# Kernel tuning notes

Hardware: AMD Instinct MI355X
Metric: run time of the kernel (lower is better)

Reference implementation:

```python
import jax, jax.numpy as jnp
import numpy as np
import math

D = 1024          # d_model = dk = dv
B = 2             # batch
T = 2048          # seq_len
F = 2 * D         # RFF feature dim
RFF_SCALE = math.sqrt(2.0 / D)
EPS = 1e-6


def setup_inputs() -> dict:
    key = jax.random.key(0)
    ks = jax.random.split(key, 6)
    s = 1.0 / math.sqrt(D)
    return {
        "x": jax.random.normal(ks[0], (B, T, D), dtype=jnp.float32),
        "Wq": jax.random.normal(ks[1], (D, D), dtype=jnp.float32) * s,
        "Wk": jax.random.normal(ks[2], (D, D), dtype=jnp.float32) * s,
        "Wv": jax.random.normal(ks[3], (D, D), dtype=jnp.float32) * s,
        "Wo": jax.random.normal(ks[4], (D, D), dtype=jnp.float32) * s,
        "omega": jax.random.normal(ks[5], (D, D), dtype=jnp.float32) * 0.5,
    }


def _rff(x, omega):
    # phi(x) = sqrt(2/m) * [cos(x @ omega), sin(x @ omega)]
    proj = x @ omega                       # (B, T, D)
    return RFF_SCALE * jnp.concatenate([jnp.cos(proj), jnp.sin(proj)], axis=-1)


def _linear_attention(Q_phi, K_phi, V):
    # Causal linear-attention recurrence over time via lax.scan.
    # S_t = S_{t-1} + phi(K_t)^T V_t ; Z_t = Z_{t-1} + phi(K_t)
    # gamma_t = (phi(Q_t) S_t) / (phi(Q_t) Z_t + eps)
    b, t, f = Q_phi.shape
    dv = V.shape[-1]
    S0 = jnp.zeros((b, f, dv), Q_phi.dtype)
    Z0 = jnp.zeros((b, f), Q_phi.dtype)

    def step(carry, inp):
        S, Z = carry
        kp, v, qp = inp                        # (B,F), (B,Dv), (B,F)
        S = S + kp[:, :, None] * v[:, None, :]  # outer-product memory update
        Z = Z + kp
        num = jnp.einsum('bf,bfd->bd', qp, S)
        den = jnp.einsum('bf,bf->b', qp, Z)
        gamma = num / (den[:, None] + EPS)
        return (S, Z), gamma

    # time-major inputs for scan
    xs = (jnp.swapaxes(K_phi, 0, 1), jnp.swapaxes(V, 0, 1), jnp.swapaxes(Q_phi, 0, 1))
    _, ys = jax.lax.scan(step, (S0, Z0), xs)   # ys: (T, B, Dv)
    return jnp.swapaxes(ys, 0, 1)              # (B, T, Dv)


def reference(x, Wq, Wk, Wv, Wo, omega):
    Q = x @ Wq
    K = x @ Wk
    V = x @ Wv
    Q_phi = _rff(Q, omega)
    K_phi = _rff(K, omega)
    y = _linear_attention(Q_phi, K_phi, V)
    return y @ Wo
```

## Files before the change

### kernel.cpp

```cpp
#include <hip/hip_runtime.h>

#define D_ 1024
#define B_ 2
#define T_ 2048
#define F_ 2048
#define CHUNK 512
#define NCHUNK 4
#define EPS_ 1e-6f
#define RSCALE 0.044194173824159216f

template<int EPI>
__global__ __launch_bounds__(256)
void sgemm128(const float* __restrict__ A, const float* __restrict__ B,
              float* __restrict__ C, int M, int N, int K, int ldc) {
    __shared__ float As[16][132];
    __shared__ float Bs[16][132];
    const int tid = threadIdx.x;
    const int bm = blockIdx.x * 128;
    const int bn = blockIdx.y * 128;
    const int tx = tid & 15, ty = tid >> 4;
    float acc[2][2][4][4] = {};
    const float* Ab = A + (size_t)bm * K;
    const float* Bb = B + bn;

    for (int k0 = 0; k0 < K; k0 += 16) {
#pragma unroll
        for (int l = 0; l < 2; ++l) {
            int idx = tid + l * 256;
            int r  = idx >> 2;
            int c4 = (idx & 3) << 2;
            float4 a = *(const float4*)(Ab + (size_t)r * K + k0 + c4);
            As[c4 + 0][r] = a.x; As[c4 + 1][r] = a.y;
            As[c4 + 2][r] = a.z; As[c4 + 3][r] = a.w;
            int rb = idx >> 5;
            int cb = (idx & 31) << 2;
            *(float4*)(&Bs[rb][cb]) = *(const float4*)(Bb + (size_t)(k0 + rb) * N + cb);
        }
        __syncthreads();
#pragma unroll
        for (int k = 0; k < 16; ++k) {
            float4 a0 = *(float4*)(&As[k][ty * 4]);
            float4 a1 = *(float4*)(&As[k][64 + ty * 4]);
            float4 b0 = *(float4*)(&Bs[k][tx * 4]);
            float4 b1 = *(float4*)(&Bs[k][64 + tx * 4]);
            float av[2][4] = {{a0.x, a0.y, a0.z, a0.w}, {a1.x, a1.y, a1.z, a1.w}};
            float bv[2][4] = {{b0.x, b0.y, b0.z, b0.w}, {b1.x, b1.y, b1.z, b1.w}};
#pragma unroll
            for (int ri = 0; ri < 2; ++ri)
#pragma unroll
                for (int i = 0; i < 4; ++i)
#pragma unroll
                    for (int ci = 0; ci < 2; ++ci)
#pragma unroll
                        for (int j = 0; j < 4; ++j)
                            acc[ri][ci][i][j] = fmaf(av[ri][i], bv[ci][j], acc[ri][ci][i][j]);
        }
        __syncthreads();
    }

#pragma unroll
    for (int ri = 0; ri < 2; ++ri)
#pragma unroll
        for (int i = 0; i < 4; ++i) {
            int R = bm + ri * 64 + ty * 4 + i;
#pragma unroll
            for (int ci = 0; ci < 2; ++ci) {
                int col = bn + ci * 64 + tx * 4;
                if (EPI == 0) {
                    float4 v = make_float4(acc[ri][ci][i][0], acc[ri][ci][i][1],
                                           acc[ri][ci][i][2], acc[ri][ci][i][3]);
                    *(float4*)(&C[(size_t)R * ldc + col]) = v;
                } else {
                    float cs[4], sn[4];
#pragma unroll
                    for (int j = 0; j < 4; ++j)
                        __sincosf(acc[ri][ci][i][j], &sn[j], &cs[j]);
                    float4 cv = make_float4(RSCALE * cs[0], RSCALE * cs[1],
                                            RSCALE * cs[2], RSCALE * cs[3]);
                    float4 sv = make_float4(RSCALE * sn[0], RSCALE * sn[1],
                                            RSCALE * sn[2], RSCALE * sn[3]);
                    *(float4*)(&C[(size_t)R * ldc + col])      = cv;
                    *(float4*)(&C[(size_t)R * ldc + col + D_]) = sv;
                }
            }
        }
}

__global__ __launch_bounds__(256)
void pall_kernel(const float* __restrict__ Qp, const float* __restrict__ Kp,
                 float* __restrict__ P) {
    const int tt = blockIdx.x >> 4, ts = blockIdx.x & 15;
    const int c = blockIdx.y, b = blockIdx.z;
    const int t0 = tt * 32, s0 = ts * 32;
    float* Pc = P + (((size_t)b * NCHUNK + c) * CHUNK) * CHUNK;
    const int tid = threadIdx.x;
    if (tt < ts) {
        int r = tid >> 3, c4 = (tid & 7) << 2;
        *(float4*)(&Pc[(size_t)(t0 + r) * CHUNK + s0 + c4]) = make_float4(0, 0, 0, 0);
        return;
    }
    __shared__ float Qs[32][36];
    __shared__ float Ks[32][36];
    const int tx = tid & 15, ty = tid >> 4;
    float acc[2][2] = {};
    const float* Qb = Qp + ((size_t)b * T_ + c * CHUNK + t0) * F_;
    const float* Kb = Kp + ((size_t)b * T_ + c * CHUNK + s0) * F_;
    for (int f0 = 0; f0 < F_; f0 += 32) {
        int r = tid >> 3, c4 = (tid & 7) << 2;
        *(float4*)(&Qs[r][c4]) = *(const float4*)(Qb + (size_t)r * F_ + f0 + c4);
        *(float4*)(&Ks[r][c4]) = *(const float4*)(Kb + (size_t)r * F_ + f0 + c4);
        __syncthreads();
#pragma unroll
        for (int k = 0; k < 32; ++k) {
            float q0 = Qs[ty * 2][k],     q1 = Qs[ty * 2 + 1][k];
            float k0v = Ks[tx * 2][k],    k1v = Ks[tx * 2 + 1][k];
            acc[0][0] = fmaf(q0, k0v, acc[0][0]);
            acc[0][1] = fmaf(q0, k1v, acc[0][1]);
            acc[1][0] = fmaf(q1, k0v, acc[1][0]);
            acc[1][1] = fmaf(q1, k1v, acc[1][1]);
        }
        __syncthreads();
    }
#pragma unroll
    for (int i = 0; i < 2; ++i)
#pragma unroll
        for (int j = 0; j < 2; ++j) {
            int t = t0 + ty * 2 + i, s = s0 + tx * 2 + j;
            Pc[(size_t)t * CHUNK + s] = (s <= t) ? acc[i][j] : 0.0f;
        }
}

__global__ __launch_bounds__(256)
void csum_kernel(const float* __restrict__ Kp, float* __restrict__ Zpre) {
    const int f = blockIdx.x * 256 + threadIdx.x;
    const int c = blockIdx.y, b = blockIdx.z;
    const float* base = Kp + ((size_t)b * T_ + c * CHUNK) * F_ + f;
    float acc = 0.f;
    for (int s = 0; s < CHUNK; ++s) acc += base[(size_t)s * F_];
    Zpre[((size_t)b * NCHUNK + c) * F_ + f] = acc;
}

__global__ __launch_bounds__(256)
void zprefix_kernel(float* __restrict__ Zpre) {
    const int f = blockIdx.x * 256 + threadIdx.x;
    const int b = blockIdx.y;
    float run = 0.f;
    for (int c = 0; c < NCHUNK; ++c) {
        size_t idx = ((size_t)b * NCHUNK + c) * F_ + f;
        float v = Zpre[idx];
        Zpre[idx] = run;
        run += v;
    }
}

__global__ __launch_bounds__(256)
void den_kernel(const float* __restrict__ Qp, const float* __restrict__ Zpre,
                const float* __restrict__ P, float* __restrict__ den) {
    const int b = blockIdx.y;
    const int w = threadIdx.x >> 6, lane = threadIdx.x & 63;
    const int t = blockIdx.x * 4 + w;
    const int c = t / CHUNK, tin = t % CHUNK;
    const float* q = Qp + ((size_t)b * T_ + t) * F_;
    const float* z = Zpre + ((size_t)b * NCHUNK + c) * F_;
    float acc = 0.f;
    for (int f = lane; f < F_; f += 64) acc = fmaf(q[f], z[f], acc);
    const float* prow = P + (((size_t)b * NCHUNK + c) * CHUNK + tin) * CHUNK;
    for (int s = lane; s < CHUNK; s += 64) acc += prow[s];
#pragma unroll
    for (int off = 32; off; off >>= 1) acc += __shfl_down(acc, off);
    if (lane == 0) den[(size_t)b * T_ + t] = acc;
}

__global__ __launch_bounds__(256)
void intra_kernel(const float* __restrict__ P, const float* __restrict__ V,
                  float* __restrict__ G) {
    const int rt = blockIdx.x >> 4, ct = blockIdx.x & 15;
    const int c = blockIdx.y, b = blockIdx.z;
    const float* Pa = P + (((size_t)b * NCHUNK + c) * CHUNK + rt * 64) * CHUNK;
    const float* Vb = V + ((size_t)b * T_ + c * CHUNK) * D_ + ct * 64;
    float* Gb = G + ((size_t)b * T_ + c * CHUNK + rt * 64) * D_ + ct * 64;
    __shared__ float As[16][68];
    __shared__ float Bs[16][68];
    const int tid = threadIdx.x, tx = tid & 15, ty = tid >> 4;
    float acc[4][4] = {};
    for (int k0 = 0; k0 < CHUNK; k0 += 16) {
        int r = tid >> 2, c4 = (tid & 3) << 2;
        float4 a = *(const float4*)(Pa + (size_t)r * CHUNK + k0 + c4);
        As[c4 + 0][r] = a.x; As[c4 + 1][r] = a.y;
        As[c4 + 2][r] = a.z; As[c4 + 3][r] = a.w;
        int rb = tid >> 4, cb = (tid & 15) << 2;
        *(float4*)(&Bs[rb][cb]) = *(const float4*)(Vb + (size_t)(k0 + rb) * D_ + cb);
        __syncthreads();
#pragma unroll
        for (int k = 0; k < 16; ++k) {
            float4 av = *(float4*)(&As[k][ty * 4]);
            float4 bv = *(float4*)(&Bs[k][tx * 4]);
            float aa[4] = {av.x, av.y, av.z, av.w};
            float bb[4] = {bv.x, bv.y, bv.z, bv.w};
#pragma unroll
            for (int i = 0; i < 4; ++i)
#pragma unroll
                for (int j = 0; j < 4; ++j)
                    acc[i][j] = fmaf(aa[i], bb[j], acc[i][j]);
        }
        __syncthreads();
    }
#pragma unroll
    for (int i = 0; i < 4; ++i)
        *(float4*)(&Gb[(size_t)(ty * 4 + i) * D_ + tx * 4]) =
            make_float4(acc[i][0], acc[i][1], acc[i][2], acc[i][3]);
}

__global__ __launch_bounds__(256)
void gamma_kernel(const float* __restrict__ Qp, const float* __restrict__ S,
                  const float* __restrict__ den, float* __restrict__ G, int c) {
    const int rt = blockIdx.x >> 4, ct = blockIdx.x & 15;
    const int b = blockIdx.y;
    const int row0 = c * CHUNK + rt * 32;
    const float* Qb = Qp + ((size_t)b * T_ + row0) * F_;
    const float* Sb = S + (size_t)b * F_ * D_ + ct * 64;
    float* Gb = G + ((size_t)b * T_ + row0) * D_ + ct * 64;
    const float* db = den + (size_t)b * T_ + row0;
    __shared__ float As[32][36];
    __shared__ float Bs[32][68];
    const int tid = threadIdx.x, tx = tid & 15, ty = tid >> 4;
    float acc[2][4] = {};
    for (int k0 = 0; k0 < F_; k0 += 32) {
        int r = tid >> 3, c4 = (tid & 7) << 2;
        float4 a = *(const float4*)(Qb + (size_t)r * F_ + k0 + c4);
        As[c4 + 0][r] = a.x; As[c4 + 1][r] = a.y;
        As[c4 + 2][r] = a.z; As[c4 + 3][r] = a.w;
#pragma unroll
        for (int l = 0; l < 2; ++l) {
            int idx = tid + l * 256;
            int rb = idx >> 4, cb = (idx & 15) << 2;
            *(float4*)(&Bs[rb][cb]) = *(const float4*)(Sb + (size_t)(k0 + rb) * D_ + cb);
        }
        __syncthreads();
#pragma unroll
        for (int k = 0; k < 32; ++k) {
            float a0 = As[k][ty * 2], a1 = As[k][ty * 2 + 1];
            float4 bv = *(float4*)(&Bs[k][tx * 4]);
            acc[0][0] = fmaf(a0, bv.x, acc[0][0]);
            acc[0][1] = fmaf(a0, bv.y, acc[0][1]);
            acc[0][2] = fmaf(a0, bv.z, acc[0][2]);
            acc[0][3] = fmaf(a0, bv.w, acc[0][3]);
            acc[1][0] = fmaf(a1, bv.x, acc[1][0]);
            acc[1][1] = fmaf(a1, bv.y, acc[1][1]);
            acc[1][2] = fmaf(a1, bv.z, acc[1][2]);
            acc[1][3] = fmaf(a1, bv.w, acc[1][3]);
        }
        __syncthreads();
    }
#pragma unroll
    for (int i = 0; i < 2; ++i) {
        int r = ty * 2 + i;
        float dd = db[r] + EPS_;
        float4 g = *(float4*)(&Gb[(size_t)r * D_ + tx * 4]);
        g.x = (acc[i][0] + g.x) / dd;
        g.y = (acc[i][1] + g.y) / dd;
        g.z = (acc[i][2] + g.z) / dd;
        g.w = (acc[i][3] + g.w) / dd;
        *(float4*)(&Gb[(size_t)r * D_ + tx * 4]) = g;
    }
}

__global__ __launch_bounds__(256)
void supd_kernel(const float* __restrict__ Kp, const float* __restrict__ V,
                 float* __restrict__ S, int c) {
    const int ft = blockIdx.x >> 4, dt = blockIdx.x & 15;
    const int b = blockIdx.y;
    const float* Kb = Kp + ((size_t)b * T_ + c * CHUNK) * F_ + ft * 64;
    const float* Vb = V + ((size_t)b * T_ + c * CHUNK) * D_ + dt * 64;
    float* Sb = S + (size_t)b * F_ * D_ + (size_t)ft * 64 * D_ + dt * 64;
    __shared__ float Ks[16][68];
    __shared__ float Vs[16][68];
    const int tid = threadIdx.x, tx = tid & 15, ty = tid >> 4;
    float acc[4][4] = {};
    for (int k0 = 0; k0 < CHUNK; k0 += 16) {
        int rb = tid >> 4, cb = (tid & 15) << 2;
        *(float4*)(&Ks[rb][cb]) = *(const float4*)(Kb + (size_t)(k0 + rb) * F_ + cb);
        *(float4*)(&Vs[rb][cb]) = *(const float4*)(Vb + (size_t)(k0 + rb) * D_ + cb);
        __syncthreads();
#pragma unroll
        for (int k = 0; k < 16; ++k) {
            float4 av = *(float4*)(&Ks[k][ty * 4]);
            float4 bv = *(float4*)(&Vs[k][tx * 4]);
            float aa[4] = {av.x, av.y, av.z, av.w};
            float bb[4] = {bv.x, bv.y, bv.z, bv.w};
#pragma unroll
            for (int i = 0; i < 4; ++i)
#pragma unroll
                for (int j = 0; j < 4; ++j)
                    acc[i][j] = fmaf(aa[i], bb[j], acc[i][j]);
        }
        __syncthreads();
    }
#pragma unroll
    for (int i = 0; i < 4; ++i) {
        float4* p = (float4*)(&Sb[(size_t)(ty * 4 + i) * D_ + tx * 4]);
        float4 s = *p;
        s.x += acc[i][0]; s.y += acc[i][1]; s.z += acc[i][2]; s.w += acc[i][3];
        *p = s;
    }
}

extern "C" void kernel_launch(void* const* d_in, const int* in_sizes, int n_in,
                              void* d_out, int out_size, void* d_ws, size_t ws_size,
                              hipStream_t stream) {
    const float* x     = (const float*)d_in[0];
    const float* Wq    = (const float*)d_in[1];
    const float* Wk    = (const float*)d_in[2];
    const float* Wv    = (const float*)d_in[3];
    const float* Wo    = (const float*)d_in[4];
    const float* omega = (const float*)d_in[5];
    float* out = (float*)d_out;
    float* ws = (float*)d_ws;

    float* Wqo   = ws;
    float* Wko   = Wqo + 1048576;
    float* V     = Wko + 1048576;
    float* Qphi  = V + 4194304;
    float* Kphi  = Qphi + 8388608;
    float* gamma = Kphi + 8388608;
    float* S     = gamma + 4194304;
    float* P     = S + 4194304;
    float* den   = P + 2097152;
    float* Zpre  = den + 4096;

    const int M = B_ * T_;

    hipMemsetAsync(S, 0, (size_t)B_ * F_ * D_ * sizeof(float), stream);

    sgemm128<0><<<dim3(8, 8), 256, 0, stream>>>(Wq, omega, Wqo, D_, D_, D_, D_);
    sgemm128<0><<<dim3(8, 8), 256, 0, stream>>>(Wk, omega, Wko, D_, D_, D_, D_);

    sgemm128<0><<<dim3(M / 128, 8), 256, 0, stream>>>(x, Wv, V, M, D_, D_, D_);
    sgemm128<1><<<dim3(M / 128, 8), 256, 0, stream>>>(x, Wqo, Qphi, M, D_, D_, F_);
    sgemm128<1><<<dim3(M / 128, 8), 256, 0, stream>>>(x, Wko, Kphi, M, D_, D_, F_);

    csum_kernel<<<dim3(F_ / 256, NCHUNK, B_), 256, 0, stream>>>(Kphi, Zpre);
    zprefix_kernel<<<dim3(F_ / 256, B_), 256, 0, stream>>>(Zpre);

    pall_kernel<<<dim3(256, NCHUNK, B_), 256, 0, stream>>>(Qphi, Kphi, P);
    den_kernel<<<dim3(T_ / 4, B_), 256, 0, stream>>>(Qphi, Zpre, P, den);
    intra_kernel<<<dim3(128, NCHUNK, B_), 256, 0, stream>>>(P, V, gamma);

    for (int c = 0; c < NCHUNK; ++c) {
        gamma_kernel<<<dim3(256, B_), 256, 0, stream>>>(Qphi, S, den, gamma, c);
        supd_kernel<<<dim3(512, B_), 256, 0, stream>>>(Kphi, V, S, c);
    }

    sgemm128<0><<<dim3(M / 128, 8), 256, 0, stream>>>(gamma, Wo, out, M, D_, D_, D_);
}
```

Baseline: 1.845 ms.

## Replace chunked recurrence with full causal-masked quadratic attention using split-bf16 MFMA

Drops the chunked S-state recurrence (intra, gamma and state-update kernels) and computes attention directly as a causal-masked phi(Q)phi(K)^T matrix multiplied by V. This runs on bf16 MFMA with a hi/lo split (three products) to approximate fp32 accuracy, and the output projection by Wo moves to the same MFMA path. Inputs are converted and transposed into split-bf16 buffers, and the work is processed per batch in a host loop. In exchange it adds conversion and transpose passes, does more FLOPs than the linear form for the full causal matrix, and gives up some precision compared with true fp32.

```diff
diff --git a/kernel.cpp b/kernel.cpp
--- a/kernel.cpp
+++ b/kernel.cpp
@@ -1,4 +1,10 @@
 #include <hip/hip_runtime.h>
+
+typedef unsigned short u16;
+typedef __attribute__((ext_vector_type(8))) short s8v;
+typedef __attribute__((ext_vector_type(4))) float f4v;
+typedef __attribute__((ext_vector_type(4))) unsigned short us4v;
+typedef __attribute__((ext_vector_type(8))) unsigned short us8v;
 
 #define D_ 1024
 #define B_ 2
@@ -8,6 +14,22 @@
 #define NCHUNK 4
 #define EPS_ 1e-6f
 #define RSCALE 0.044194173824159216f
+
+__device__ __forceinline__ u16 bf16h(float a) {
+    unsigned u = __float_as_uint(a);
+    return (u16)((u + 0x7fffu + ((u >> 16) & 1u)) >> 16);
+}
+__device__ __forceinline__ float bf2f(u16 h) {
+    return __uint_as_float(((unsigned)h) << 16);
+}
+__device__ __forceinline__ void bsplit2(float a, u16& h, u16& l) {
+    h = bf16h(a);
+    l = bf16h(a - bf2f(h));
+}
+
+#define GLOAD16(gp, lp) __builtin_amdgcn_global_load_lds( \
+    (const __attribute__((address_space(1))) unsigned int*)(gp), \
+    (__attribute__((address_space(3))) unsigned int*)(lp), 16, 0, 0)
 
 template<int EPI>
 __global__ __launch_bounds__(256)
@@ -171,138 +193,148 @@
     if (lane == 0) den[(size_t)b * T_ + t] = acc;
 }
 
-__global__ __launch_bounds__(256)
-void intra_kernel(const float* __restrict__ P, const float* __restrict__ V,
-                  float* __restrict__ G) {
-    const int rt = blockIdx.x >> 4, ct = blockIdx.x & 15;
-    const int c = blockIdx.y, b = blockIdx.z;
-    const float* Pa = P + (((size_t)b * NCHUNK + c) * CHUNK + rt * 64) * CHUNK;
-    const float* Vb = V + ((size_t)b * T_ + c * CHUNK) * D_ + ct * 64;
-    float* Gb = G + ((size_t)b * T_ + c * CHUNK + rt * 64) * D_ + ct * 64;
-    __shared__ float As[16][68];
-    __shared__ float Bs[16][68];
-    const int tid = threadIdx.x, tx = tid & 15, ty = tid >> 4;
-    float acc[4][4] = {};
-    for (int k0 = 0; k0 < CHUNK; k0 += 16) {
-        int r = tid >> 2, c4 = (tid & 3) << 2;
-        float4 a = *(const float4*)(Pa + (size_t)r * CHUNK + k0 + c4);
-        As[c4 + 0][r] = a.x; As[c4 + 1][r] = a.y;
-        As[c4 + 2][r] = a.z; As[c4 + 3][r] = a.w;
-        int rb = tid >> 4, cb = (tid & 15) << 2;
-        *(float4*)(&Bs[rb][cb]) = *(const float4*)(Vb + (size_t)(k0 + rb) * D_ + cb);
-        __syncthreads();
-#pragma unroll
-        for (int k = 0; k < 16; ++k) {
-            float4 av = *(float4*)(&As[k][ty * 4]);
-            float4 bv = *(float4*)(&Bs[k][tx * 4]);
-            float aa[4] = {av.x, av.y, av.z, av.w};
-            float bb[4] = {bv.x, bv.y, bv.z, bv.w};
+template<int EPI>
+__global__ __launch_bounds__(256)
+void mgemm2(const u16* __restrict__ A0, const u16* __restrict__ A1,
+            const u16* __restrict__ B0, const u16* __restrict__ B1,
+            int K, float* __restrict__ Cf, u16* __restrict__ O0,
+            u16* __restrict__ O1, const float* __restrict__ dptr, int ldo) {
+    __shared__ u16 lds[4 * 4096];
+    const int tid = threadIdx.x;
+    const int bm = blockIdx.x * 128, bn = blockIdx.y * 128;
+
+    if (EPI == 3 && bm + 128 <= bn) {
+        us8v zz = {0, 0, 0, 0, 0, 0, 0, 0};
+#pragma unroll
+        for (int i = 0; i < 8; ++i) {
+            int j = i * 256 + tid;
+            int r = j >> 4, c8 = (j & 15) * 8;
+            size_t o = (size_t)(bm + r) * ldo + bn + c8;
+            *(us8v*)&O0[o] = zz;
+            *(us8v*)&O1[o] = zz;
+        }
+        return;
+    }
+
+    const int kend = (EPI == 5) ? (bm + 128 < K ? bm + 128 : K) : K;
+
+    const int wv = tid >> 6, lane = tid & 63;
+    const int wr = (wv >> 1) * 64, wc = (wv & 1) * 64;
+    const int lr = lane & 15, kb = lane >> 4;
+
+    f4v acc[4][4] = {};
+
+    const int sr0 = tid >> 2, sc0 = (tid & 3) * 8;
+    const int sl0 = tid * 8, sl1 = (tid + 256) * 8;
+
+    for (int k0 = 0; k0 < kend; k0 += 32) {
+        size_t ga0 = (size_t)(bm + sr0) * K + k0 + sc0;
+        size_t ga1 = ga0 + (size_t)64 * K;
+        size_t gb0 = (size_t)(bn + sr0) * K + k0 + sc0;
+        size_t gb1 = gb0 + (size_t)64 * K;
+        GLOAD16(A0 + ga0, lds + 0 * 4096 + sl0);
+        GLOAD16(A0 + ga1, lds + 0 * 4096 + sl1);
+        GLOAD16(A1 + ga0, lds + 1 * 4096 + sl0);
+        GLOAD16(A1 + ga1, lds + 1 * 4096 + sl1);
+        GLOAD16(B0 + gb0, lds + 2 * 4096 + sl0);
+        GLOAD16(B0 + gb1, lds + 2 * 4096 + sl1);
+        GLOAD16(B1 + gb0, lds + 3 * 4096 + sl0);
+        GLOAD16(B1 + gb1, lds + 3 * 4096 + sl1);
+        __syncthreads();
+
+        constexpr int TA[3] = {0, 0, 1};
+        constexpr int TB[3] = {0, 1, 0};
+#pragma unroll
+        for (int t = 0; t < 3; ++t) {
+            const u16* la = lds + TA[t] * 4096;
+            const u16* lb = lds + (2 + TB[t]) * 4096;
+            s8v af[4], bfr[4];
+#pragma unroll
+            for (int i = 0; i < 4; ++i) {
+                af[i]  = *(const s8v*)&la[(wr + i * 16 + lr) * 32 + kb * 8];
+                bfr[i] = *(const s8v*)&lb[(wc + i * 16 + lr) * 32 + kb * 8];
+            }
 #pragma unroll
             for (int i = 0; i < 4; ++i)
 #pragma unroll
                 for (int j = 0; j < 4; ++j)
-                    acc[i][j] = fmaf(aa[i], bb[j], acc[i][j]);
-        }
-        __syncthreads();
-    }
-#pragma unroll
-    for (int i = 0; i < 4; ++i)
-        *(float4*)(&Gb[(size_t)(ty * 4 + i) * D_ + tx * 4]) =
-            make_float4(acc[i][0], acc[i][1], acc[i][2], acc[i][3]);
-}
-
-__global__ __launch_bounds__(256)
-void gamma_kernel(const float* __restrict__ Qp, const float* __restrict__ S,
-                  const float* __restrict__ den, float* __restrict__ G, int c) {
-    const int rt = blockIdx.x >> 4, ct = blockIdx.x & 15;
-    const int b = blockIdx.y;
-    const int row0 = c * CHUNK + rt * 32;
-    const float* Qb = Qp + ((size_t)b * T_ + row0) * F_;
-    const float* Sb = S + (size_t)b * F_ * D_ + ct * 64;
-    float* Gb = G + ((size_t)b * T_ + row0) * D_ + ct * 64;
-    const float* db = den + (size_t)b * T_ + row0;
-    __shared__ float As[32][36];
-    __shared__ float Bs[32][68];
-    const int tid = threadIdx.x, tx = tid & 15, ty = tid >> 4;
-    float acc[2][4] = {};
-    for (int k0 = 0; k0 < F_; k0 += 32) {
-        int r = tid >> 3, c4 = (tid & 7) << 2;
-        float4 a = *(const float4*)(Qb + (size_t)r * F_ + k0 + c4);
-        As[c4 + 0][r] = a.x; As[c4 + 1][r] = a.y;
-        As[c4 + 2][r] = a.z; As[c4 + 3][r] = a.w;
-#pragma unroll
-        for (int l = 0; l < 2; ++l) {
-            int idx = tid + l * 256;
-            int rb = idx >> 4, cb = (idx & 15) << 2;
-            *(float4*)(&Bs[rb][cb]) = *(const float4*)(Sb + (size_t)(k0 + rb) * D_ + cb);
-        }
-        __syncthreads();
-#pragma unroll
-        for (int k = 0; k < 32; ++k) {
-            float a0 = As[k][ty * 2], a1 = As[k][ty * 2 + 1];
-            float4 bv = *(float4*)(&Bs[k][tx * 4]);
-            acc[0][0] = fmaf(a0, bv.x, acc[0][0]);
-            acc[0][1] = fmaf(a0, bv.y, acc[0][1]);
-            acc[0][2] = fmaf(a0, bv.z, acc[0][2]);
-            acc[0][3] = fmaf(a0, bv.w, acc[0][3]);
-            acc[1][0] = fmaf(a1, bv.x, acc[1][0]);
-            acc[1][1] = fmaf(a1, bv.y, acc[1][1]);
-            acc[1][2] = fmaf(a1, bv.z, acc[1][2]);
-            acc[1][3] = fmaf(a1, bv.w, acc[1][3]);
-        }
-        __syncthreads();
-    }
-#pragma unroll
-    for (int i = 0; i < 2; ++i) {
-        int r = ty * 2 + i;
-        float dd = db[r] + EPS_;
-        float4 g = *(float4*)(&Gb[(size_t)r * D_ + tx * 4]);
-        g.x = (acc[i][0] + g.x) / dd;
-        g.y = (acc[i][1] + g.y) / dd;
-        g.z = (acc[i][2] + g.z) / dd;
-        g.w = (acc[i][3] + g.w) / dd;
-        *(float4*)(&Gb[(size_t)r * D_ + tx * 4]) = g;
-    }
-}
-
-__global__ __launch_bounds__(256)
-void supd_kernel(const float* __restrict__ Kp, const float* __restrict__ V,
-                 float* __restrict__ S, int c) {
-    const int ft = blockIdx.x >> 4, dt = blockIdx.x & 15;
-    const int b = blockIdx.y;
-    const float* Kb = Kp + ((size_t)b * T_ + c * CHUNK) * F_ + ft * 64;
-    const float* Vb = V + ((size_t)b * T_ + c * CHUNK) * D_ + dt * 64;
-    float* Sb = S + (size_t)b * F_ * D_ + (size_t)ft * 64 * D_ + dt * 64;
-    __shared__ float Ks[16][68];
-    __shared__ float Vs[16][68];
-    const int tid = threadIdx.x, tx = tid & 15, ty = tid >> 4;
-    float acc[4][4] = {};
-    for (int k0 = 0; k0 < CHUNK; k0 += 16) {
-        int rb = tid >> 4, cb = (tid & 15) << 2;
-        *(float4*)(&Ks[rb][cb]) = *(const float4*)(Kb + (size_t)(k0 + rb) * F_ + cb);
-        *(float4*)(&Vs[rb][cb]) = *(const float4*)(Vb + (size_t)(k0 + rb) * D_ + cb);
-        __syncthreads();
-#pragma unroll
-        for (int k = 0; k < 16; ++k) {
-            float4 av = *(float4*)(&Ks[k][ty * 4]);
-            float4 bv = *(float4*)(&Vs[k][tx * 4]);
-            float aa[4] = {av.x, av.y, av.z, av.w};
-            float bb[4] = {bv.x, bv.y, bv.z, bv.w};
-#pragma unroll
-            for (int i = 0; i < 4; ++i)
-#pragma unroll
-                for (int j = 0; j < 4; ++j)
-                    acc[i][j] = fmaf(aa[i], bb[j], acc[i][j]);
-        }
-        __syncthreads();
-    }
+                    acc[i][j] = __builtin_amdgcn_mfma_f32_16x16x32_bf16(
+                        af[i], bfr[j], acc[i][j], 0, 0, 0);
+        }
+        __syncthreads();
+    }
+
+    const int rbase = bm + wr + kb * 4;
+    const int cbase = bn + wc + lr;
 #pragma unroll
     for (int i = 0; i < 4; ++i) {
-        float4* p = (float4*)(&Sb[(size_t)(ty * 4 + i) * D_ + tx * 4]);
-        float4 s = *p;
-        s.x += acc[i][0]; s.y += acc[i][1]; s.z += acc[i][2]; s.w += acc[i][3];
-        *p = s;
-    }
+        const int R0 = rbase + i * 16;
+#pragma unroll
+        for (int j = 0; j < 4; ++j) {
+            const int Cc = cbase + j * 16;
+            f4v v = acc[i][j];
+            if (EPI == 0) {
+#pragma unroll
+                for (int q = 0; q < 4; ++q)
+                    Cf[(size_t)(R0 + q) * ldo + Cc] = v[q];
+            } else if (EPI == 3) {
+#pragma unroll
+                for (int q = 0; q < 4; ++q) {
+                    int t = R0 + q;
+                    float val = (Cc <= t) ? v[q] : 0.0f;
+                    u16 h, l; bsplit2(val, h, l);
+                    size_t o = (size_t)t * ldo + Cc;
+                    O0[o] = h; O1[o] = l;
+                }
+            } else if (EPI == 5) {
+#pragma unroll
+                for (int q = 0; q < 4; ++q) {
+                    float g = v[q] / (dptr[R0 + q] + EPS_);
+                    u16 h, l; bsplit2(g, h, l);
+                    size_t o = (size_t)(R0 + q) * ldo + Cc;
+                    O0[o] = h; O1[o] = l;
+                }
+            }
+        }
+    }
+}
+
+__global__ __launch_bounds__(256)
+void convk2(const float* __restrict__ in, u16* __restrict__ o0,
+            u16* __restrict__ o1, int n4) {
+    int i = blockIdx.x * 256 + threadIdx.x;
+    if (i >= n4) return;
+    float4 v = ((const float4*)in)[i];
+    us4v p0, p1;
+    float vv[4] = {v.x, v.y, v.z, v.w};
+#pragma unroll
+    for (int q = 0; q < 4; ++q) {
+        u16 h, l; bsplit2(vv[q], h, l);
+        p0[q] = h; p1[q] = l;
+    }
+    ((us4v*)o0)[i] = p0;
+    ((us4v*)o1)[i] = p1;
+}
+
+__global__ __launch_bounds__(256)
+void tpc(const float* __restrict__ in, u16* __restrict__ oh,
+         u16* __restrict__ ol, int inW, int outW) {
+    __shared__ float t[32][33];
+    const int r = threadIdx.x >> 3, c4 = (threadIdx.x & 7) << 2;
+    const int row0 = blockIdx.y * 32, col0 = blockIdx.x * 32;
+    float4 v = *(const float4*)&in[(size_t)(row0 + r) * inW + col0 + c4];
+    t[r][c4 + 0] = v.x; t[r][c4 + 1] = v.y;
+    t[r][c4 + 2] = v.z; t[r][c4 + 3] = v.w;
+    __syncthreads();
+    us4v h4, l4;
+#pragma unroll
+    for (int i = 0; i < 4; ++i) {
+        u16 h, l; bsplit2(t[c4 + i][r], h, l);
+        h4[i] = h; l4[i] = l;
+    }
+    size_t o = (size_t)(col0 + r) * outW + row0 + c4;
+    *(us4v*)&oh[o] = h4;
+    *(us4v*)&ol[o] = l4;
 }
 
 extern "C" void kernel_launch(void* const* d_in, const int* in_sizes, int n_in,
@@ -315,41 +347,53 @@
     const float* Wo    = (const float*)d_in[4];
     const float* omega = (const float*)d_in[5];
     float* out = (float*)d_out;
-    float* ws = (float*)d_ws;
-
-    float* Wqo   = ws;
-    float* Wko   = Wqo + 1048576;
-    float* V     = Wko + 1048576;
-    float* Qphi  = V + 4194304;
-    float* Kphi  = Qphi + 8388608;
-    float* gamma = Kphi + 8388608;
-    float* S     = gamma + 4194304;
-    float* P     = S + 4194304;
-    float* den   = P + 2097152;
-    float* Zpre  = den + 4096;
-
-    const int M = B_ * T_;
-
-    hipMemsetAsync(S, 0, (size_t)B_ * F_ * D_ * sizeof(float), stream);
+
+    char* WS = (char*)d_ws;
+    float* Wqo = (float*)(WS + 0);
+    float* Wko = (float*)(WS + 4194304);
+    u16*  WoTh = (u16*)(WS + 8388608);
+    u16*  WoTl = (u16*)(WS + 10485760);
+    float* den = (float*)(WS + 12582912);
+    float* Zpre = (float*)(WS + 12599296);
+    float* Qf  = (float*)(WS + 13631488);
+    float* Kf  = (float*)(WS + 30408704);
+    float* Vf  = (float*)(WS + 47185920);
+    float* Pd  = (float*)(WS + 55574528);
+    u16* Qph = (u16*)(WS + 59768832);
+    u16* Qpl = (u16*)(WS + 68157440);
+    u16* Kph = (u16*)(WS + 76546048);
+    u16* Kpl = (u16*)(WS + 84934656);
+    u16* VTh = (u16*)(WS + 93323264);
+    u16* VTl = (u16*)(WS + 97517568);
+    u16* P2h = (u16*)(WS + 101711872);
+    u16* P2l = (u16*)(WS + 110100480);
+    u16* g2h = (u16*)(WS + 118489088);
+    u16* g2l = (u16*)(WS + 122683392);
 
     sgemm128<0><<<dim3(8, 8), 256, 0, stream>>>(Wq, omega, Wqo, D_, D_, D_, D_);
     sgemm128<0><<<dim3(8, 8), 256, 0, stream>>>(Wk, omega, Wko, D_, D_, D_, D_);
-
-    sgemm128<0><<<dim3(M / 128, 8), 256, 0, stream>>>(x, Wv, V, M, D_, D_, D_);
-    sgemm128<1><<<dim3(M / 128, 8), 256, 0, stream>>>(x, Wqo, Qphi, M, D_, D_, F_);
-    sgemm128<1><<<dim3(M / 128, 8), 256, 0, stream>>>(x, Wko, Kphi, M, D_, D_, F_);
-
-    csum_kernel<<<dim3(F_ / 256, NCHUNK, B_), 256, 0, stream>>>(Kphi, Zpre);
-    zprefix_kernel<<<dim3(F_ / 256, B_), 256, 0, stream>>>(Zpre);
-
-    pall_kernel<<<dim3(256, NCHUNK, B_), 256, 0, stream>>>(Qphi, Kphi, P);
-    den_kernel<<<dim3(T_ / 4, B_), 256, 0, stream>>>(Qphi, Zpre, P, den);
-    intra_kernel<<<dim3(128, NCHUNK, B_), 256, 0, stream>>>(P, V, gamma);
-
-    for (int c = 0; c < NCHUNK; ++c) {
-        gamma_kernel<<<dim3(256, B_), 256, 0, stream>>>(Qphi, S, den, gamma, c);
-        supd_kernel<<<dim3(512, B_), 256, 0, stream>>>(Kphi, V, S, c);
-    }
-
-    sgemm128<0><<<dim3(M / 128, 8), 256, 0, stream>>>(gamma, Wo, out, M, D_, D_, D_);
-}
+    tpc<<<dim3(32, 32), 256, 0, stream>>>(Wo, WoTh, WoTl, 1024, 1024);
+
+    for (int b = 0; b < 2; ++b) {
+        const float* xb = x + (size_t)b * T_ * D_;
+        sgemm128<1><<<dim3(16, 8), 256, 0, stream>>>(xb, Wqo, Qf, T_, D_, D_, F_);
+        sgemm128<1><<<dim3(16, 8), 256, 0, stream>>>(xb, Wko, Kf, T_, D_, D_, F_);
+        sgemm128<0><<<dim3(16, 8), 256, 0, stream>>>(xb, Wv, Vf, T_, D_, D_, D_);
+        csum_kernel<<<dim3(8, 4, 1), 256, 0, stream>>>(Kf, Zpre);
+        zprefix_kernel<<<dim3(8, 1), 256, 0, stream>>>(Zpre);
+        pall_kernel<<<dim3(256, 4, 1), 256, 0, stream>>>(Qf, Kf, Pd);
+        den_kernel<<<dim3(512, 1), 256, 0, stream>>>(Qf, Zpre, Pd, den + b * T_);
+
+        convk2<<<4096, 256, 0, stream>>>(Qf, Qph, Qpl, 1048576);
+        convk2<<<4096, 256, 0, stream>>>(Kf, Kph, Kpl, 1048576);
+        tpc<<<dim3(32, 64), 256, 0, stream>>>(Vf, VTh, VTl, 1024, 2048);
+
+        mgemm2<3><<<dim3(16, 16), 256, 0, stream>>>(
+            Qph, Qpl, Kph, Kpl, 2048, nullptr, P2h, P2l, nullptr, 2048);
+        mgemm2<5><<<dim3(16, 8), 256, 0, stream>>>(
+            P2h, P2l, VTh, VTl, 2048, nullptr, g2h, g2l, den + b * T_, 1024);
+        mgemm2<0><<<dim3(16, 8), 256, 0, stream>>>(
+            g2h, g2l, WoTh, WoTl, 1024, out + (size_t)b * T_ * D_,
+            nullptr, nullptr, nullptr, 1024);
+    }
+}
```

Measured after the change: 1.860 ms. Within noise of the previous version (+0.8%).
